# Kernel optimization log

Hardware: AMD Instinct MI355X
Metric: run time of the kernel (lower is better)

Reference implementation:

```python
import jax, jax.numpy as jnp
import numpy as np

B, T, E, NH = 2, 1024, 512, 8


def setup_inputs() -> dict:
    key = jax.random.key(0)
    ks = jax.random.split(key, 7)
    s = 0.02
    return {
        "x": jax.random.normal(ks[0], (B, T, E), dtype=jnp.float32),
        "W_qkv": jax.random.normal(ks[1], (E, 3 * E), dtype=jnp.float32) * s,
        "b_qkv": jax.random.normal(ks[2], (3 * E,), dtype=jnp.float32) * s,
        "W_od": jax.random.normal(ks[3], (E, 2 * NH), dtype=jnp.float32) * s,
        "b_od": jax.random.normal(ks[4], (2 * NH,), dtype=jnp.float32) * s,
        "W_out": jax.random.normal(ks[5], (E, E), dtype=jnp.float32) * s,
        "b_out": jax.random.normal(ks[6], (E,), dtype=jnp.float32) * s,
        "length": T,
    }


def reference(x, W_qkv, b_qkv, W_od, b_od, W_out, b_out, length):
    b, t, e = x.shape
    nh = W_od.shape[1] // 2
    hd = e // nh
    scaling = float(hd) ** (-0.5)

    qkv = x @ W_qkv + b_qkv
    Q, K, V = jnp.split(qkv, 3, axis=-1)  # each (b, t, e)

    od = Q @ W_od + b_od  # (b, t, 2*nh)
    offset, duration = jnp.split(od, 2, axis=-1)
    offset = jnp.tanh(offset) * length
    duration = jax.nn.sigmoid(duration) * length

    qidx = jnp.arange(length, dtype=x.dtype)[None, :, None]  # (1, t, 1)
    anchor = qidx + offset  # (b, t, nh)

    # 'b t nh -> (b nh) t'
    anchor = anchor.transpose(0, 2, 1).reshape(b * nh, t)
    duration = duration.transpose(0, 2, 1).reshape(b * nh, t)

    start = anchor - duration
    end = anchor + duration
    bl = jnp.floor(start)          # left bound index
    br = jnp.ceil(end)             # right bound index
    al = jnp.floor(anchor)         # anchor left index
    ar = al + 1                    # anchor right index
    dist_al = anchor - al          # anchor_dist_l

    r = jnp.arange(length, dtype=x.dtype)[None, None, :]  # (1, 1, t)

    def pmask(idx):  # point mask (bnh, t, t), float
        return (r == idx[:, :, None]).astype(x.dtype)

    point_weight = (1.0
                    + (bl - start)[:, :, None] * pmask(bl)
                    + (end - br)[:, :, None] * pmask(br)
                    + dist_al[:, :, None] * pmask(ar)
                    + (1.0 - dist_al)[:, :, None] * pmask(al))

    attn_mask = (r < bl[:, :, None]) | (r > br[:, :, None])  # (bnh, t, t) bool

    def heads(z):  # 'b t (nh hd) -> (b nh) t hd'
        return z.reshape(b, t, nh, hd).transpose(0, 2, 1, 3).reshape(b * nh, t, hd)

    Qh, Kh, Vh = heads(Q), heads(K), heads(V)

    scores = jnp.einsum('bic,brc->bir', Qh, Kh) * scaling
    scores = scores * point_weight
    scores = jnp.where(attn_mask, jnp.asarray(-1e8, x.dtype), scores)
    attn = jax.nn.softmax(scores, axis=-1)

    out = jnp.einsum('bir,brc->bic', attn, Vh)  # (bnh, t, hd)
    out = out.reshape(b, nh, t, hd).transpose(0, 2, 1, 3).reshape(b, t, e)
    return out @ W_out + b_out
```

## Files before the change

### kernel.cpp

```cpp
#include <hip/hip_runtime.h>

typedef unsigned short ushort_t;
typedef short s16x8 __attribute__((ext_vector_type(8)));
typedef short s16x4 __attribute__((ext_vector_type(4)));
typedef float f32x4 __attribute__((ext_vector_type(4)));

#if defined(__HIP_DEVICE_COMPILE__)
#define MFMA16(a, b, c) __builtin_amdgcn_mfma_f32_16x16x16bf16_1k(a, b, c, 0, 0, 0)
#else
__device__ __host__ static inline f32x4 MFMA16(s16x4, s16x4, f32x4 c) { return c; }
#endif

#define DEVINL __device__ __forceinline__

DEVINL void gload_lds16(const void* g, void* l) {
#if defined(__HIP_DEVICE_COMPILE__)
  __builtin_amdgcn_global_load_lds((const __attribute__((address_space(1))) void*)g,
                                   (__attribute__((address_space(3))) void*)l,
                                   16, 0, 0);
#endif
}

DEVINL ushort_t f2b(float f) {
  union { float f; unsigned int u; } v; v.f = f;
  unsigned int r = (v.u + 0x7fffu + ((v.u >> 16) & 1u)) >> 16;
  return (ushort_t)r;
}

DEVINL ushort_t f2b_hw(float f) {
  union { __bf16 h; ushort_t u; } cv;
  cv.h = (__bf16)f;
  return cv.u;
}

__global__ __launch_bounds__(256) void prep_kernel(
    const float* __restrict__ Wqkv, const float* __restrict__ bq,
    const float* __restrict__ Wod, const float* __restrict__ bod,
    const float* __restrict__ Wout, const float* __restrict__ x,
    ushort_t* __restrict__ WqkvT, ushort_t* __restrict__ WoT,
    float* __restrict__ Wcomb, float* __restrict__ bcomb,
    ushort_t* __restrict__ xbf)
{
  __shared__ ushort_t tile[64 * 72];
  const int b = blockIdx.x;
  const int tid = threadIdx.x;

  if (b < 256) {
    const float* in;
    ushort_t* out;
    int N, bx, by;
    if (b < 192) { in = Wqkv; out = WqkvT; N = 1536; bx = b % 24; by = b / 24; }
    else         { in = Wout; out = WoT;   N = 512;  bx = (b - 192) % 8; by = (b - 192) / 8; }
    const int K = 512;
    const int n0 = bx * 64, k0 = by * 64;
    const int cr = tid >> 4;
    const int cc = (tid & 15) * 4;
#pragma unroll
    for (int p = 0; p < 4; p++) {
      int k = k0 + p * 16 + cr;
      float4 v = *(const float4*)(in + k * N + n0 + cc);
      ushort4 o; o.x = f2b(v.x); o.y = f2b(v.y); o.z = f2b(v.z); o.w = f2b(v.w);
      *(ushort4*)(tile + (p * 16 + cr) * 72 + cc) = o;
    }
    __syncthreads();
#pragma unroll
    for (int p = 0; p < 4; p++) {
      int n = n0 + p * 16 + cr;
      ushort4 v;
      v.x = tile[(cc + 0) * 72 + p * 16 + cr];
      v.y = tile[(cc + 1) * 72 + p * 16 + cr];
      v.z = tile[(cc + 2) * 72 + p * 16 + cr];
      v.w = tile[(cc + 3) * 72 + p * 16 + cr];
      *(ushort4*)(out + n * K + k0 + cc) = v;
    }
    return;
  }

  if (b >= 385) {
    const int base = (b - 385) * 2048 + tid * 8;
    float4 v0 = *(const float4*)(x + base);
    float4 v1 = *(const float4*)(x + base + 4);
    s16x8 o;
    o[0] = (short)f2b_hw(v0.x); o[1] = (short)f2b_hw(v0.y);
    o[2] = (short)f2b_hw(v0.z); o[3] = (short)f2b_hw(v0.w);
    o[4] = (short)f2b_hw(v1.x); o[5] = (short)f2b_hw(v1.y);
    o[6] = (short)f2b_hw(v1.z); o[7] = (short)f2b_hw(v1.w);
    *(s16x8*)(xbf + base) = o;
    return;
  }

  const int w = tid >> 6, lane = tid & 63;
  const int c = (b - 256) * 4 + w;
  if (c > 512) return;
  float a[8];
  const float* src = (c < 512) ? (Wqkv + c * 1536 + lane * 8) : (bq + lane * 8);
  float4 a0 = *(const float4*)(src);
  float4 a1 = *(const float4*)(src + 4);
  a[0]=a0.x; a[1]=a0.y; a[2]=a0.z; a[3]=a0.w;
  a[4]=a1.x; a[5]=a1.y; a[6]=a1.z; a[7]=a1.w;

  float s[16];
#pragma unroll
  for (int j = 0; j < 16; j++) s[j] = 0.f;
#pragma unroll
  for (int i = 0; i < 8; i++) {
    const float* wp = Wod + (lane * 8 + i) * 16;
#pragma unroll
    for (int j = 0; j < 16; j++) s[j] += a[i] * wp[j];
  }
#pragma unroll
  for (int mask = 1; mask < 64; mask <<= 1)
#pragma unroll
    for (int j = 0; j < 16; j++) s[j] += __shfl_xor(s[j], mask);

  if (lane < 16) {
    if (c < 512) Wcomb[c * 16 + lane] = s[lane];
    else         bcomb[lane] = s[lane] + bod[lane];
  }
}

__global__ __launch_bounds__(256) void qkv_od_kernel(
    const float* __restrict__ x, const ushort_t* __restrict__ xbf,
    const ushort_t* __restrict__ WT,
    const float* __restrict__ bqkv,
    const float* __restrict__ Wcomb, const float* __restrict__ bcomb,
    const int* __restrict__ lenp,
    ushort_t* __restrict__ Qh, ushort_t* __restrict__ Kh, ushort_t* __restrict__ VT,
    float* __restrict__ params)
{
  const int blk = blockIdx.x;
  const int tid = threadIdx.x;

  if (blk >= 384) {
    const int w = tid >> 6, lane = tid & 63;
    const int m = (blk - 384) * 4 + w;
    int li = lenp[0];
    float len = (li > 0 && li < 1048576) ? (float)li : 1024.0f;

    const float* qp = x + m * 512 + lane * 8;
    float q[8];
    float4 qa = *(const float4*)(qp);
    float4 qb = *(const float4*)(qp + 4);
    q[0]=qa.x; q[1]=qa.y; q[2]=qa.z; q[3]=qa.w;
    q[4]=qb.x; q[5]=qb.y; q[6]=qb.z; q[7]=qb.w;

    float s[16];
#pragma unroll
    for (int j = 0; j < 16; j++) s[j] = 0.f;
#pragma unroll
    for (int i = 0; i < 8; i++) {
      const float* wp = Wcomb + (lane * 8 + i) * 16;
#pragma unroll
      for (int j = 0; j < 16; j++) s[j] += q[i] * wp[j];
    }
#pragma unroll
    for (int mask = 1; mask < 64; mask <<= 1)
#pragma unroll
      for (int j = 0; j < 16; j++) s[j] += __shfl_xor(s[j], mask);

    if (lane < 8) {
      int h = lane;
      int bb = m >> 10, t = m & 1023;
      float odo = s[h] + bcomb[h];
      float odd = s[8 + h] + bcomb[8 + h];
      float offset = tanhf(odo) * len;
      float dur = len / (1.f + expf(-odd));
      float anchor = (float)t + offset;
      float start = anchor - dur, end = anchor + dur;
      float bl = floorf(start), br = ceilf(end);
      float al = floorf(anchor);
      float da = anchor - al;
      float* pp = params + ((bb * 8 + h) * 1024 + t) * 6;
      pp[0] = bl; pp[1] = br; pp[2] = al;
      pp[3] = bl - start; pp[4] = end - br; pp[5] = da;
    }
    return;
  }

  __shared__ __align__(16) ushort_t As[64 * 32];
  __shared__ __align__(16) ushort_t Bs[128 * 32];
  const int lane = tid & 63, w = tid >> 6;
  const int wr = w >> 1, wc = w & 1;
  const int quad = lane >> 4, l16 = lane & 15;
  const int bx = blk % 12, by = blk / 12;
  const int m0 = by * 64, n0 = bx * 128;

  f32x4 acc[2][4];
#pragma unroll
  for (int i = 0; i < 2; i++)
#pragma unroll
    for (int j = 0; j < 4; j++) acc[i][j] = f32x4{0.f, 0.f, 0.f, 0.f};

  const int idx = tid * 8;
  const int ra = idx >> 5, ca = idx & 31;
  const int rb1 = (idx + 2048) >> 5, cb1 = (idx + 2048) & 31;
  const int wbase = w << 10;
  char* asb  = (char*)As + wbase;
  char* bsb0 = (char*)Bs + wbase;
  char* bsb1 = (char*)Bs + 4096 + wbase;
  const ushort_t* ga  = xbf + (m0 + ra) * 512 + ca;
  const ushort_t* gb0 = WT + (n0 + ra) * 512 + ca;
  const ushort_t* gb1 = WT + (n0 + rb1) * 512 + cb1;

  for (int k0 = 0; k0 < 512; k0 += 32) {
    __syncthreads();
    gload_lds16(ga + k0, asb);
    gload_lds16(gb0 + k0, bsb0);
    gload_lds16(gb1 + k0, bsb1);
    __syncthreads();

    s16x8 af[2], bfr[4];
#pragma unroll
    for (int mt = 0; mt < 2; mt++)
      af[mt] = *(const s16x8*)(As + (wr * 32 + mt * 16 + l16) * 32 + quad * 8);
#pragma unroll
    for (int nt = 0; nt < 4; nt++)
      bfr[nt] = *(const s16x8*)(Bs + (wc * 64 + nt * 16 + l16) * 32 + quad * 8);
#pragma unroll
    for (int mt = 0; mt < 2; mt++)
#pragma unroll
      for (int nt = 0; nt < 4; nt++)
        acc[mt][nt] = __builtin_amdgcn_mfma_f32_16x16x32_bf16(af[mt], bfr[nt], acc[mt][nt], 0, 0, 0);
  }

#pragma unroll
  for (int nt = 0; nt < 4; nt++) {
    int c = n0 + wc * 64 + nt * 16 + l16;
    float bias = bqkv[c];
    int which = c >> 9;
    int e = c & 511;
    int h = e >> 6, d = e & 63;
#pragma unroll
    for (int mt = 0; mt < 2; mt++) {
      int mbase = m0 + wr * 32 + mt * 16 + quad * 4;
      int bb = mbase >> 10, t = mbase & 1023;
      int bh = bb * 8 + h;
      if (which == 2) {
        ushort4 pk;
        pk.x = f2b(acc[mt][nt][0] + bias);
        pk.y = f2b(acc[mt][nt][1] + bias);
        pk.z = f2b(acc[mt][nt][2] + bias);
        pk.w = f2b(acc[mt][nt][3] + bias);
        *(ushort4*)(VT + (bh * 64 + d) * 1024 + t) = pk;
      } else {
        ushort_t* dst = (which == 0) ? Qh : Kh;
        float sc = (which == 0) ? 0.125f : 1.0f;
#pragma unroll
        for (int rr = 0; rr < 4; rr++)
          dst[(bh * 1024 + t + rr) * 64 + d] = f2b((acc[mt][nt][rr] + bias) * sc);
      }
    }
  }
}

__global__ __launch_bounds__(256, 4) void attn_kernel(
    const ushort_t* __restrict__ Qh, const ushort_t* __restrict__ Kh,
    const ushort_t* __restrict__ VT, const float* __restrict__ params,
    ushort_t* __restrict__ Oh)
{
  constexpr int TS = 64 * 72;
  __shared__ __align__(16) ushort_t KV[4 * TS];

  const int tid = threadIdx.x;
  const int lane = tid & 63, wc = tid >> 6;
  const int quad = lane >> 4, l16 = lane & 15;
  const int bh = blockIdx.x;
  const int mrow = blockIdx.y * 16;

  const float* ppl = params + (bh * 1024 + mrow + l16) * 6;
  float bl = ppl[0], br = ppl[1], al = ppl[2];
  float wl = ppl[3], wr2 = ppl[4], da = ppl[5];
  bool empty = (br < 0.f) || (bl > 1023.f);
  float lo = empty ? 0.f    : fmaxf(bl, 0.f);
  float hi = empty ? 1023.f : fminf(br, 1023.f);
#pragma unroll
  for (int mask = 1; mask < 16; mask <<= 1) {
    lo = fminf(lo, __shfl_xor(lo, mask));
    hi = fmaxf(hi, __shfl_xor(hi, mask));
  }
  const int tlo = ((int)lo) >> 6, thi = ((int)hi) >> 6;

  const ushort_t* qrow = Qh + (bh * 1024 + mrow + l16) * 64;
  s16x4 bq[4];
#pragma unroll
  for (int i = 0; i < 4; i++)
    bq[i] = *(const s16x4*)(qrow + i * 16 + quad * 4);

  float lr = 0.f;
  f32x4 Oacc[4];
#pragma unroll
  for (int g = 0; g < 4; g++) Oacc[g] = f32x4{0.f, 0.f, 0.f, 0.f};

  const int srow = tid >> 2, sseg = (tid & 3) * 16;
  const ushort_t* kgb = Kh + (bh * 1024 + srow) * 64 + sseg;
  const ushort_t* vgb = VT + (bh * 64 + srow) * 1024 + sseg;

  s16x8 kr0, kr1, vr0, vr1;
  {
    const int r0 = tlo * 64;
    kr0 = *(const s16x8*)(kgb + r0 * 64);
    kr1 = *(const s16x8*)(kgb + r0 * 64 + 8);
    vr0 = *(const s16x8*)(vgb + r0);
    vr1 = *(const s16x8*)(vgb + r0 + 8);
  }
  {
    ushort_t* Kt = KV;
    ushort_t* Vt = KV + TS;
    *(s16x8*)(Kt + srow * 72 + sseg)     = kr0;
    *(s16x8*)(Kt + srow * 72 + sseg + 8) = kr1;
    *(s16x8*)(Vt + srow * 72 + sseg)     = vr0;
    *(s16x8*)(Vt + srow * 72 + sseg + 8) = vr1;
  }
  __syncthreads();

  for (int tt = tlo; tt <= thi; tt++) {
    const int p = (tt - tlo) & 1;
    ushort_t* Ktp = KV + p * 2 * TS;
    ushort_t* Vtp = KV + p * 2 * TS + TS;
    const int r0 = tt * 64;
    const bool more = (tt + 1 <= thi);

    if (more) {
      const int r1 = (tt + 1) * 64;
      kr0 = *(const s16x8*)(kgb + r1 * 64);
      kr1 = *(const s16x8*)(kgb + r1 * 64 + 8);
      vr0 = *(const s16x8*)(vgb + r1);
      vr1 = *(const s16x8*)(vgb + r1 + 8);
    }

    const ushort_t* krow = Ktp + (wc * 16 + l16) * 72;
    f32x4 z = {0.f, 0.f, 0.f, 0.f};
#pragma unroll
    for (int i = 0; i < 4; i++) {
      s16x4 ak = *(const s16x4*)(krow + i * 16 + quad * 4);
      z = MFMA16(ak, bq[i], z);
    }

    const int cbase = r0 + wc * 16;
    const float c0f = (float)cbase, c1f = c0f + 15.f;
    bool f = (bl < c0f) && (br > c1f) && ((al + 1.f < c0f) || (al > c1f));
    s16x4 pt;
    if (__all((int)f)) {
#pragma unroll
      for (int rr = 0; rr < 4; rr++) {
        float pv = __expf(z[rr]);
        lr += pv;
        pt[rr] = (short)f2b_hw(pv);
      }
    } else {
#pragma unroll
      for (int rr = 0; rr < 4; rr++) {
        float cf = (float)(cbase + quad * 4 + rr);
        float s = z[rr];
        float wgt = 1.f;
        wgt += (cf == bl) ? wl : 0.f;
        wgt += (cf == br) ? wr2 : 0.f;
        wgt += (cf == al + 1.f) ? da : 0.f;
        wgt += (cf == al) ? (1.f - da) : 0.f;
        s *= wgt;
        s = (cf < bl || cf > br) ? -30.f : s;
        float pv = __expf(s);
        lr += pv;
        pt[rr] = (short)f2b_hw(pv);
      }
    }

#pragma unroll
    for (int g = 0; g < 4; g++) {
      s16x4 av = *(const s16x4*)(Vtp + (g * 16 + l16) * 72 + wc * 16 + quad * 4);
      Oacc[g] = MFMA16(av, pt, Oacc[g]);
    }

    if (more) {
      ushort_t* Ktn = KV + (p ^ 1) * 2 * TS;
      ushort_t* Vtn = KV + (p ^ 1) * 2 * TS + TS;
      *(s16x8*)(Ktn + srow * 72 + sseg)     = kr0;
      *(s16x8*)(Ktn + srow * 72 + sseg + 8) = kr1;
      *(s16x8*)(Vtn + srow * 72 + sseg)     = vr0;
      *(s16x8*)(Vtn + srow * 72 + sseg + 8) = vr1;
      __syncthreads();
    }
  }

  lr += __shfl_xor(lr, 16);
  lr += __shfl_xor(lr, 32);

  __syncthreads();
  float* Om  = (float*)KV;
  float* lwf = Om + 64 * 65;
#pragma unroll
  for (int g = 0; g < 4; g++)
#pragma unroll
    for (int rr = 0; rr < 4; rr++)
      Om[(wc * 16 + l16) * 65 + g * 16 + quad * 4 + rr] = Oacc[g][rr];
  if (quad == 0) lwf[wc * 16 + l16] = lr;
  __syncthreads();

  const int bb = bh >> 3, h = bh & 7;
  {
    int e = tid;
#pragma unroll
    for (int it = 0; it < 4; it++, e += 256) {
      int r = e >> 6, col = e & 63;
      float lg = lwf[r] + lwf[16 + r] + lwf[32 + r] + lwf[48 + r];
      float o  = Om[r * 65 + col] + Om[(16 + r) * 65 + col]
               + Om[(32 + r) * 65 + col] + Om[(48 + r) * 65 + col];
      int t = mrow + r;
      Oh[((bb << 10) + t) * 512 + h * 64 + col] = f2b_hw(o / lg);
    }
  }
}

__global__ __launch_bounds__(256) void out_gemm_kernel(
    const ushort_t* __restrict__ Oh, const ushort_t* __restrict__ WT,
    const float* __restrict__ bout, float* __restrict__ outp)
{
  __shared__ __align__(16) ushort_t As[64 * 32];
  __shared__ __align__(16) ushort_t Bs[64 * 32];
  const int tid = threadIdx.x;
  const int lane = tid & 63, w = tid >> 6;
  const int wr = w >> 1, wc = w & 1;
  const int quad = lane >> 4, l16 = lane & 15;
  const int m0 = blockIdx.y * 64, n0 = blockIdx.x * 64;

  f32x4 acc[2][2];
#pragma unroll
  for (int i = 0; i < 2; i++)
#pragma unroll
    for (int j = 0; j < 2; j++) acc[i][j] = f32x4{0.f, 0.f, 0.f, 0.f};

  const int idx = tid * 8;
  const int ra = idx >> 5, ca = idx & 31;
  const int wbase = w << 10;
  char* asb = (char*)As + wbase;
  char* bsb = (char*)Bs + wbase;
  const ushort_t* ga = Oh + (m0 + ra) * 512 + ca;
  const ushort_t* gb = WT + (n0 + ra) * 512 + ca;

  for (int k0 = 0; k0 < 512; k0 += 32) {
    __syncthreads();
    gload_lds16(ga + k0, asb);
    gload_lds16(gb + k0, bsb);
    __syncthreads();

    s16x8 af[2], bfr[2];
#pragma unroll
    for (int mt = 0; mt < 2; mt++)
      af[mt] = *(const s16x8*)(As + (wr * 32 + mt * 16 + l16) * 32 + quad * 8);
#pragma unroll
    for (int nt = 0; nt < 2; nt++)
      bfr[nt] = *(const s16x8*)(Bs + (wc * 32 + nt * 16 + l16) * 32 + quad * 8);
#pragma unroll
    for (int mt = 0; mt < 2; mt++)
#pragma unroll
      for (int nt = 0; nt < 2; nt++)
        acc[mt][nt] = __builtin_amdgcn_mfma_f32_16x16x32_bf16(af[mt], bfr[nt], acc[mt][nt], 0, 0, 0);
  }

#pragma unroll
  for (int nt = 0; nt < 2; nt++) {
    int c = n0 + wc * 32 + nt * 16 + l16;
    float bias = bout[c];
#pragma unroll
    for (int mt = 0; mt < 2; mt++) {
#pragma unroll
      for (int rr = 0; rr < 4; rr++) {
        int m = m0 + wr * 32 + mt * 16 + quad * 4 + rr;
        outp[m * 512 + c] = acc[mt][nt][rr] + bias;
      }
    }
  }
}

extern "C" void kernel_launch(void* const* d_in, const int* in_sizes, int n_in,
                              void* d_out, int out_size, void* d_ws, size_t ws_size,
                              hipStream_t stream)
{
  const float* x    = (const float*)d_in[0];
  const float* Wqkv = (const float*)d_in[1];
  const float* bqkv = (const float*)d_in[2];
  const float* Wod  = (const float*)d_in[3];
  const float* bod  = (const float*)d_in[4];
  const float* Wout = (const float*)d_in[5];
  const float* bout = (const float*)d_in[6];
  const int* lenp   = (const int*)d_in[7];

  char* ws = (char*)d_ws;
  ushort_t* WqkvT  = (ushort_t*)(ws);
  ushort_t* WoT    = (ushort_t*)(ws + 1572864);
  ushort_t* Qh     = (ushort_t*)(ws + 4194304);
  ushort_t* Kh     = (ushort_t*)(ws + 6291456);
  ushort_t* VT     = (ushort_t*)(ws + 8388608);
  ushort_t* Oh     = (ushort_t*)(ws + 10485760);
  float*    Wcomb  = (float*)(ws + 12582912);
  float*    bcomb  = (float*)(ws + 12615680);
  float*    params = (float*)(ws + 12615744);
  ushort_t* xbf    = (ushort_t*)(ws + 13008960);

  prep_kernel<<<897, 256, 0, stream>>>(Wqkv, bqkv, Wod, bod, Wout, x,
                                       WqkvT, WoT, Wcomb, bcomb, xbf);
  qkv_od_kernel<<<896, 256, 0, stream>>>(x, xbf, WqkvT, bqkv, Wcomb, bcomb, lenp,
                                         Qh, Kh, VT, params);
  attn_kernel<<<dim3(16, 64), 256, 0, stream>>>(Qh, Kh, VT, params, Oh);
  out_gemm_kernel<<<dim3(8, 32), 256, 0, stream>>>(Oh, WoT, bout, (float*)d_out);
}
```

Before: 124.4 us.

## Load K/V fragments directly into registers and drop LDS staging in attention

The attention kernel no longer stages K and V tiles through double-buffered shared memory. Each wave now loads its own K and V MFMA operands straight from global memory into registers, prefetching the next tile, and the QK product uses the 16x16x32 bf16 MFMA. Removing the per-tile barriers and LDS round-trips also shrinks LDS use, so occupancy is raised to 6 blocks per CU and s_setprio is wrapped around the MFMA groups. The cost is uncoalesced, strided global reads, mainly the V loads, which depend on the cache to avoid extra memory traffic.

```diff
diff --git a/kernel.cpp b/kernel.cpp
--- a/kernel.cpp
+++ b/kernel.cpp
@@ -10,6 +10,7 @@
 #else
 __device__ __host__ static inline f32x4 MFMA16(s16x4, s16x4, f32x4 c) { return c; }
 #endif
+#define MFMA32(a, b, c) __builtin_amdgcn_mfma_f32_16x16x32_bf16(a, b, c, 0, 0, 0)
 
 #define DEVINL __device__ __forceinline__
 
@@ -253,14 +254,12 @@
   }
 }
 
-__global__ __launch_bounds__(256, 4) void attn_kernel(
+__global__ __launch_bounds__(256, 6) void attn_kernel(
     const ushort_t* __restrict__ Qh, const ushort_t* __restrict__ Kh,
     const ushort_t* __restrict__ VT, const float* __restrict__ params,
     ushort_t* __restrict__ Oh)
 {
-  constexpr int TS = 64 * 72;
-  __shared__ __align__(16) ushort_t KV[4 * TS];
-
+  __shared__ __align__(16) float Om[64 * 65 + 64];
   const int tid = threadIdx.x;
   const int lane = tid & 63, wc = tid >> 6;
   const int quad = lane >> 4, l16 = lane & 15;
@@ -281,62 +280,45 @@
   const int tlo = ((int)lo) >> 6, thi = ((int)hi) >> 6;
 
   const ushort_t* qrow = Qh + (bh * 1024 + mrow + l16) * 64;
-  s16x4 bq[4];
-#pragma unroll
-  for (int i = 0; i < 4; i++)
-    bq[i] = *(const s16x4*)(qrow + i * 16 + quad * 4);
+  s16x8 bq0 = *(const s16x8*)(qrow + quad * 8);
+  s16x8 bq1 = *(const s16x8*)(qrow + 32 + quad * 8);
 
   float lr = 0.f;
   f32x4 Oacc[4];
 #pragma unroll
   for (int g = 0; g < 4; g++) Oacc[g] = f32x4{0.f, 0.f, 0.f, 0.f};
 
-  const int srow = tid >> 2, sseg = (tid & 3) * 16;
-  const ushort_t* kgb = Kh + (bh * 1024 + srow) * 64 + sseg;
-  const ushort_t* vgb = VT + (bh * 64 + srow) * 1024 + sseg;
-
-  s16x8 kr0, kr1, vr0, vr1;
-  {
-    const int r0 = tlo * 64;
-    kr0 = *(const s16x8*)(kgb + r0 * 64);
-    kr1 = *(const s16x8*)(kgb + r0 * 64 + 8);
-    vr0 = *(const s16x8*)(vgb + r0);
-    vr1 = *(const s16x8*)(vgb + r0 + 8);
-  }
-  {
-    ushort_t* Kt = KV;
-    ushort_t* Vt = KV + TS;
-    *(s16x8*)(Kt + srow * 72 + sseg)     = kr0;
-    *(s16x8*)(Kt + srow * 72 + sseg + 8) = kr1;
-    *(s16x8*)(Vt + srow * 72 + sseg)     = vr0;
-    *(s16x8*)(Vt + srow * 72 + sseg + 8) = vr1;
-  }
-  __syncthreads();
+  const ushort_t* kptr = Kh + (bh * 1024 + tlo * 64 + wc * 16 + l16) * 64 + quad * 8;
+  const ushort_t* vptr = VT + (bh * 64 + l16) * 1024 + tlo * 64 + wc * 16 + quad * 4;
+
+  s16x8 ck0 = *(const s16x8*)(kptr);
+  s16x8 ck1 = *(const s16x8*)(kptr + 32);
+  s16x4 cv0 = *(const s16x4*)(vptr);
+  s16x4 cv1 = *(const s16x4*)(vptr + 16384);
+  s16x4 cv2 = *(const s16x4*)(vptr + 32768);
+  s16x4 cv3 = *(const s16x4*)(vptr + 49152);
 
   for (int tt = tlo; tt <= thi; tt++) {
-    const int p = (tt - tlo) & 1;
-    ushort_t* Ktp = KV + p * 2 * TS;
-    ushort_t* Vtp = KV + p * 2 * TS + TS;
-    const int r0 = tt * 64;
-    const bool more = (tt + 1 <= thi);
-
+    const bool more = (tt < thi);
+    s16x8 nk0, nk1;
+    s16x4 nv0, nv1, nv2, nv3;
     if (more) {
-      const int r1 = (tt + 1) * 64;
-      kr0 = *(const s16x8*)(kgb + r1 * 64);
-      kr1 = *(const s16x8*)(kgb + r1 * 64 + 8);
-      vr0 = *(const s16x8*)(vgb + r1);
-      vr1 = *(const s16x8*)(vgb + r1 + 8);
-    }
-
-    const ushort_t* krow = Ktp + (wc * 16 + l16) * 72;
+      nk0 = *(const s16x8*)(kptr + 4096);
+      nk1 = *(const s16x8*)(kptr + 4096 + 32);
+      nv0 = *(const s16x4*)(vptr + 64);
+      nv1 = *(const s16x4*)(vptr + 64 + 16384);
+      nv2 = *(const s16x4*)(vptr + 64 + 32768);
+      nv3 = *(const s16x4*)(vptr + 64 + 49152);
+    }
+    kptr += 4096; vptr += 64;
+
     f32x4 z = {0.f, 0.f, 0.f, 0.f};
-#pragma unroll
-    for (int i = 0; i < 4; i++) {
-      s16x4 ak = *(const s16x4*)(krow + i * 16 + quad * 4);
-      z = MFMA16(ak, bq[i], z);
-    }
-
-    const int cbase = r0 + wc * 16;
+    __builtin_amdgcn_s_setprio(1);
+    z = MFMA32(ck0, bq0, z);
+    z = MFMA32(ck1, bq1, z);
+    __builtin_amdgcn_s_setprio(0);
+
+    const int cbase = tt * 64 + wc * 16;
     const float c0f = (float)cbase, c1f = c0f + 15.f;
     bool f = (bl < c0f) && (br > c1f) && ((al + 1.f < c0f) || (al > c1f));
     s16x4 pt;
@@ -365,28 +347,22 @@
       }
     }
 
-#pragma unroll
-    for (int g = 0; g < 4; g++) {
-      s16x4 av = *(const s16x4*)(Vtp + (g * 16 + l16) * 72 + wc * 16 + quad * 4);
-      Oacc[g] = MFMA16(av, pt, Oacc[g]);
-    }
+    __builtin_amdgcn_s_setprio(1);
+    Oacc[0] = MFMA16(cv0, pt, Oacc[0]);
+    Oacc[1] = MFMA16(cv1, pt, Oacc[1]);
+    Oacc[2] = MFMA16(cv2, pt, Oacc[2]);
+    Oacc[3] = MFMA16(cv3, pt, Oacc[3]);
+    __builtin_amdgcn_s_setprio(0);
 
     if (more) {
-      ushort_t* Ktn = KV + (p ^ 1) * 2 * TS;
-      ushort_t* Vtn = KV + (p ^ 1) * 2 * TS + TS;
-      *(s16x8*)(Ktn + srow * 72 + sseg)     = kr0;
-      *(s16x8*)(Ktn + srow * 72 + sseg + 8) = kr1;
-      *(s16x8*)(Vtn + srow * 72 + sseg)     = vr0;
-      *(s16x8*)(Vtn + srow * 72 + sseg + 8) = vr1;
-      __syncthreads();
+      ck0 = nk0; ck1 = nk1;
+      cv0 = nv0; cv1 = nv1; cv2 = nv2; cv3 = nv3;
     }
   }
 
   lr += __shfl_xor(lr, 16);
   lr += __shfl_xor(lr, 32);
 
-  __syncthreads();
-  float* Om  = (float*)KV;
   float* lwf = Om + 64 * 65;
 #pragma unroll
   for (int g = 0; g < 4; g++)
```

Measured after the change: 150.9 us. 1.21x slower.

## Share K/V tiles across 32 query rows per attention block

Applied to the files above, without the earlier changes.

The attention kernel now runs 512 threads per block and covers 32 query rows (two groups of four waves) instead of 16, so each K/V tile staged in shared memory serves twice as many queries. The key-tile range per block becomes the union of both groups' bands, combined through a small shared array and an extra barrier. Each thread now does one 16-byte K load and one V load per tile instead of two of each. The final reduction is reindexed over eight waves. The intent is to halve global K/V traffic per query. In exchange the block scans a possibly wider band and launches half as many blocks with more threads each.

```diff
diff --git a/kernel.cpp b/kernel.cpp
--- a/kernel.cpp
+++ b/kernel.cpp
@@ -253,21 +253,25 @@
   }
 }
 
-__global__ __launch_bounds__(256, 4) void attn_kernel(
+__global__ __launch_bounds__(512, 4) void attn_kernel(
     const ushort_t* __restrict__ Qh, const ushort_t* __restrict__ Kh,
     const ushort_t* __restrict__ VT, const float* __restrict__ params,
     ushort_t* __restrict__ Oh)
 {
   constexpr int TS = 64 * 72;
   __shared__ __align__(16) ushort_t KV[4 * TS];
+  __shared__ float band[16];
 
   const int tid = threadIdx.x;
-  const int lane = tid & 63, wc = tid >> 6;
+  const int lane = tid & 63, w = tid >> 6;
+  const int wq = w >> 2;
+  const int wc = w & 3;
   const int quad = lane >> 4, l16 = lane & 15;
   const int bh = blockIdx.x;
-  const int mrow = blockIdx.y * 16;
-
-  const float* ppl = params + (bh * 1024 + mrow + l16) * 6;
+  const int mrow = blockIdx.y * 32;
+  const int qidx = mrow + wq * 16 + l16;
+
+  const float* ppl = params + (bh * 1024 + qidx) * 6;
   float bl = ppl[0], br = ppl[1], al = ppl[2];
   float wl = ppl[3], wr2 = ppl[4], da = ppl[5];
   bool empty = (br < 0.f) || (bl > 1023.f);
@@ -278,9 +282,17 @@
     lo = fminf(lo, __shfl_xor(lo, mask));
     hi = fmaxf(hi, __shfl_xor(hi, mask));
   }
-  const int tlo = ((int)lo) >> 6, thi = ((int)hi) >> 6;
-
-  const ushort_t* qrow = Qh + (bh * 1024 + mrow + l16) * 64;
+  if (lane == 0) { band[w * 2] = lo; band[w * 2 + 1] = hi; }
+  __syncthreads();
+  float blo = band[0], bhi = band[1];
+#pragma unroll
+  for (int i = 1; i < 8; i++) {
+    blo = fminf(blo, band[i * 2]);
+    bhi = fmaxf(bhi, band[i * 2 + 1]);
+  }
+  const int tlo = ((int)blo) >> 6, thi = ((int)bhi) >> 6;
+
+  const ushort_t* qrow = Qh + (bh * 1024 + qidx) * 64;
   s16x4 bq[4];
 #pragma unroll
   for (int i = 0; i < 4; i++)
@@ -291,25 +303,21 @@
 #pragma unroll
   for (int g = 0; g < 4; g++) Oacc[g] = f32x4{0.f, 0.f, 0.f, 0.f};
 
-  const int srow = tid >> 2, sseg = (tid & 3) * 16;
+  const int srow = tid >> 3, sseg = (tid & 7) * 8;
   const ushort_t* kgb = Kh + (bh * 1024 + srow) * 64 + sseg;
   const ushort_t* vgb = VT + (bh * 64 + srow) * 1024 + sseg;
 
-  s16x8 kr0, kr1, vr0, vr1;
+  s16x8 kr, vr;
   {
     const int r0 = tlo * 64;
-    kr0 = *(const s16x8*)(kgb + r0 * 64);
-    kr1 = *(const s16x8*)(kgb + r0 * 64 + 8);
-    vr0 = *(const s16x8*)(vgb + r0);
-    vr1 = *(const s16x8*)(vgb + r0 + 8);
+    kr = *(const s16x8*)(kgb + r0 * 64);
+    vr = *(const s16x8*)(vgb + r0);
   }
   {
     ushort_t* Kt = KV;
     ushort_t* Vt = KV + TS;
-    *(s16x8*)(Kt + srow * 72 + sseg)     = kr0;
-    *(s16x8*)(Kt + srow * 72 + sseg + 8) = kr1;
-    *(s16x8*)(Vt + srow * 72 + sseg)     = vr0;
-    *(s16x8*)(Vt + srow * 72 + sseg + 8) = vr1;
+    *(s16x8*)(Kt + srow * 72 + sseg) = kr;
+    *(s16x8*)(Vt + srow * 72 + sseg) = vr;
   }
   __syncthreads();
 
@@ -322,10 +330,8 @@
 
     if (more) {
       const int r1 = (tt + 1) * 64;
-      kr0 = *(const s16x8*)(kgb + r1 * 64);
-      kr1 = *(const s16x8*)(kgb + r1 * 64 + 8);
-      vr0 = *(const s16x8*)(vgb + r1);
-      vr1 = *(const s16x8*)(vgb + r1 + 8);
+      kr = *(const s16x8*)(kgb + r1 * 64);
+      vr = *(const s16x8*)(vgb + r1);
     }
 
     const ushort_t* krow = Ktp + (wc * 16 + l16) * 72;
@@ -374,10 +380,8 @@
     if (more) {
       ushort_t* Ktn = KV + (p ^ 1) * 2 * TS;
       ushort_t* Vtn = KV + (p ^ 1) * 2 * TS + TS;
-      *(s16x8*)(Ktn + srow * 72 + sseg)     = kr0;
-      *(s16x8*)(Ktn + srow * 72 + sseg + 8) = kr1;
-      *(s16x8*)(Vtn + srow * 72 + sseg)     = vr0;
-      *(s16x8*)(Vtn + srow * 72 + sseg + 8) = vr1;
+      *(s16x8*)(Ktn + srow * 72 + sseg) = kr;
+      *(s16x8*)(Vtn + srow * 72 + sseg) = vr;
       __syncthreads();
     }
   }
@@ -387,24 +391,26 @@
 
   __syncthreads();
   float* Om  = (float*)KV;
-  float* lwf = Om + 64 * 65;
+  float* lwf = Om + 8 * 16 * 65;
 #pragma unroll
   for (int g = 0; g < 4; g++)
 #pragma unroll
     for (int rr = 0; rr < 4; rr++)
-      Om[(wc * 16 + l16) * 65 + g * 16 + quad * 4 + rr] = Oacc[g][rr];
-  if (quad == 0) lwf[wc * 16 + l16] = lr;
+      Om[(w * 16 + l16) * 65 + g * 16 + quad * 4 + rr] = Oacc[g][rr];
+  if (quad == 0) lwf[w * 16 + l16] = lr;
   __syncthreads();
 
   const int bb = bh >> 3, h = bh & 7;
   {
     int e = tid;
 #pragma unroll
-    for (int it = 0; it < 4; it++, e += 256) {
+    for (int it = 0; it < 4; it++, e += 512) {
       int r = e >> 6, col = e & 63;
-      float lg = lwf[r] + lwf[16 + r] + lwf[32 + r] + lwf[48 + r];
-      float o  = Om[r * 65 + col] + Om[(16 + r) * 65 + col]
-               + Om[(32 + r) * 65 + col] + Om[(48 + r) * 65 + col];
+      int p0 = (r >> 4) * 4, rl = r & 15;
+      float lg = lwf[(p0 + 0) * 16 + rl] + lwf[(p0 + 1) * 16 + rl]
+               + lwf[(p0 + 2) * 16 + rl] + lwf[(p0 + 3) * 16 + rl];
+      float o  = Om[((p0 + 0) * 16 + rl) * 65 + col] + Om[((p0 + 1) * 16 + rl) * 65 + col]
+               + Om[((p0 + 2) * 16 + rl) * 65 + col] + Om[((p0 + 3) * 16 + rl) * 65 + col];
       int t = mrow + r;
       Oh[((bb << 10) + t) * 512 + h * 64 + col] = f2b_hw(o / lg);
     }
@@ -501,6 +507,6 @@
                                        WqkvT, WoT, Wcomb, bcomb, xbf);
   qkv_od_kernel<<<896, 256, 0, stream>>>(x, xbf, WqkvT, bqkv, Wcomb, bcomb, lenp,
                                          Qh, Kh, VT, params);
-  attn_kernel<<<dim3(16, 64), 256, 0, stream>>>(Qh, Kh, VT, params, Oh);
+  attn_kernel<<<dim3(16, 32), 512, 0, stream>>>(Qh, Kh, VT, params, Oh);
   out_gemm_kernel<<<dim3(8, 32), 256, 0, stream>>>(Oh, WoT, bout, (float*)d_out);
 }
```

Result: no change. 123.1 us (-1.1%).
